# Performance work log

Hardware: AMD Instinct MI355X
Metric: run time of the kernel (lower is better)

## Reference

```python
import jax, jax.numpy as jnp
import numpy as np

LENGTH_OF_SIGNAL = 2560
OUTLIER_THRESHOLD = 3.0


def setup_inputs() -> dict:
    key = jax.random.key(0)
    inputs = jax.random.normal(key, (16384, 2560, 1), dtype=jnp.float32)
    return {"inputs": inputs}


def reference(inputs):
    # inputs: (B, S, 1). All stats reduce over the sequence axis (dim=1).
    B, S, _ = inputs.shape
    x = inputs[..., 0]  # (B, S)

    mean = jnp.mean(x, axis=1)                       # (B,)
    maximum = jnp.max(x, axis=1)
    minimum = jnp.min(x, axis=1)
    p2p = maximum - minimum
    rms = jnp.sqrt(jnp.mean(x * x, axis=1))
    var = jnp.var(x, axis=1, ddof=1)                 # torch.var is unbiased
    std = jnp.sqrt(var)                              # torch.std is unbiased

    centered = x - mean[:, None]
    skewness = jnp.mean(centered ** 3, axis=1) / (std ** 3)
    kurtosis = jnp.mean(centered ** 4, axis=1) / (std ** 4)

    abs_x = jnp.abs(x)
    abs_sum = jnp.sum(abs_x, axis=1)
    abs_max = jnp.max(abs_x, axis=1)
    shape_factor = rms * LENGTH_OF_SIGNAL / abs_sum
    impulse_factor = abs_max * LENGTH_OF_SIGNAL / abs_sum

    outliers = jnp.sum(
        (jnp.abs(centered) > OUTLIER_THRESHOLD * std[:, None]).astype(jnp.int32),
        axis=1,
    ).astype(jnp.float32)

    # zero-crossing rate on flattened (B, S) signal
    zcr = jnp.sum(
        (jnp.diff(jnp.sign(x), axis=1) != 0).astype(jnp.float32), axis=1
    ) / (2.0 * S)

    # Hjorth parameters (activity, mobility, complexity)
    d1 = jnp.diff(x, axis=1)
    d2 = jnp.diff(d1, axis=1)
    var_d1 = jnp.var(d1, axis=1, ddof=1)
    var_d2 = jnp.var(d2, axis=1, ddof=1)
    activity = var
    mobility = jnp.sqrt(var_d1 / var)
    complexity = jnp.sqrt(var_d2 / var_d1)

    stacked = jnp.stack(
        [mean, maximum, minimum, p2p, var, rms, skewness, kurtosis,
         shape_factor, impulse_factor, outliers, zcr,
         activity, mobility, complexity],
        axis=1,
    )  # (B, 15)
    return stacked
```

## Files before the change

kernel.cpp:

```cpp
#include <hip/hip_runtime.h>
#include <math.h>


typedef float f32x2 __attribute__((ext_vector_type(2)));
typedef float f32x4 __attribute__((ext_vector_type(4)));

constexpr int S_LEN = 2560;
constexpr int NROWS = 16384;

#define DPP_ADD_F32(x, ctrl) do { \
    int t_ = __builtin_amdgcn_update_dpp(0, __float_as_int(x), ctrl, 0xf, 0xf, false); \
    x += __int_as_float(t_); } while (0)
#define DPP_MAX_F32(x, ctrl) do { \
    int t_ = __builtin_amdgcn_update_dpp(__float_as_int(x), __float_as_int(x), ctrl, 0xf, 0xf, false); \
    x = fmaxf(x, __int_as_float(t_)); } while (0)
#define DPP_MIN_F32(x, ctrl) do { \
    int t_ = __builtin_amdgcn_update_dpp(__float_as_int(x), __float_as_int(x), ctrl, 0xf, 0xf, false); \
    x = fminf(x, __int_as_float(t_)); } while (0)

__device__ __forceinline__ float wave_sum_f32(float x) {
    DPP_ADD_F32(x, 0x111); DPP_ADD_F32(x, 0x112); DPP_ADD_F32(x, 0x114);
    DPP_ADD_F32(x, 0x118); DPP_ADD_F32(x, 0x142); DPP_ADD_F32(x, 0x143);
    return x;
}
__device__ __forceinline__ float wave_max_f32(float x) {
    DPP_MAX_F32(x, 0x111); DPP_MAX_F32(x, 0x112); DPP_MAX_F32(x, 0x114);
    DPP_MAX_F32(x, 0x118); DPP_MAX_F32(x, 0x142); DPP_MAX_F32(x, 0x143);
    return x;
}
__device__ __forceinline__ float wave_min_f32(float x) {
    DPP_MIN_F32(x, 0x111); DPP_MIN_F32(x, 0x112); DPP_MIN_F32(x, 0x114);
    DPP_MIN_F32(x, 0x118); DPP_MIN_F32(x, 0x142); DPP_MIN_F32(x, 0x143);
    return x;
}
__device__ __forceinline__ double wave_sum_f64(double x) {
#define DPP_ADD_F64(ctrl) do { \
    long long b_ = __double_as_longlong(x); \
    int lo_ = __builtin_amdgcn_update_dpp(0, (int)(b_ & 0xffffffffLL), ctrl, 0xf, 0xf, false); \
    int hi_ = __builtin_amdgcn_update_dpp(0, (int)(b_ >> 32), ctrl, 0xf, 0xf, false); \
    x += __longlong_as_double(((long long)hi_ << 32) | (unsigned int)lo_); } while (0)
    DPP_ADD_F64(0x111); DPP_ADD_F64(0x112); DPP_ADD_F64(0x114);
    DPP_ADD_F64(0x118); DPP_ADD_F64(0x142); DPP_ADD_F64(0x143);
#undef DPP_ADD_F64
    return x;
}
__device__ __forceinline__ double readlane_f64(double x, int l) {
    long long b = __double_as_longlong(x);
    int lo = __builtin_amdgcn_readlane((int)(b & 0xffffffffLL), l);
    int hi = __builtin_amdgcn_readlane((int)(b >> 32), l);
    return __longlong_as_double(((long long)hi << 32) | (unsigned int)lo);
}

__global__ __launch_bounds__(256, 8)
void health_pass1(const float* __restrict__ in, float* __restrict__ ws) {
    __shared__ double Lsum[4], Lsq[4];
    __shared__ float  Lnb[2][2];

    const int lane = threadIdx.x & 63;
    const int wid  = threadIdx.x >> 6;
    const int hidx = wid & 1;
    const int rsl  = wid >> 1;
    const int row  = blockIdx.x * 2 + rsl;

    const f32x4* rp = reinterpret_cast<const f32x4*>(in)
                    + (size_t)row * (S_LEN / 4) + hidx * (1280 / 4) + lane;

    f32x4 X[5];
#pragma unroll
    for (int k = 0; k < 5; ++k) X[k] = rp[k * 64];

    f32x2 sp = {0.f, 0.f}, qp = {0.f, 0.f}, sabsp = {0.f, 0.f};
    f32x2 vmaxp = {-INFINITY, -INFINITY}, vminp = {INFINITY, INFINITY};
#pragma unroll
    for (int k = 0; k < 5; ++k) {
        f32x2 lo = __builtin_shufflevector(X[k], X[k], 0, 1);
        f32x2 hi = __builtin_shufflevector(X[k], X[k], 2, 3);
        sp += lo + hi;
        qp = __builtin_elementwise_fma(lo, lo, qp);
        qp = __builtin_elementwise_fma(hi, hi, qp);
        sabsp += __builtin_elementwise_max(lo, -lo);
        sabsp += __builtin_elementwise_max(hi, -hi);
        vmaxp = __builtin_elementwise_max(vmaxp, __builtin_elementwise_max(lo, hi));
        vminp = __builtin_elementwise_min(vminp, __builtin_elementwise_min(lo, hi));
    }

    const double sum_l = (double)sp.x + (double)sp.y;
    const double sq_l  = (double)qp.x + (double)qp.y;
    const double sum_u = readlane_f64(wave_sum_f64(sum_l), 63);
    const double sq_u  = readlane_f64(wave_sum_f64(sq_l), 63);

    float sabs = wave_sum_f32(sabsp.x + sabsp.y);
    float vmax = wave_max_f32(fmaxf(vmaxp.x, vmaxp.y));
    float vmin = wave_min_f32(fminf(vminp.x, vminp.y));

    if (lane == 0) {
        Lsum[wid] = sum_u;  Lsq[wid] = sq_u;
        if (hidx == 1) { Lnb[rsl][0] = X[0][0]; Lnb[rsl][1] = X[0][1]; }
    }
    __syncthreads();
    const double tsum = Lsum[rsl * 2] + Lsum[rsl * 2 + 1];
    const double tsq  = Lsq[rsl * 2]  + Lsq[rsl * 2 + 1];

    const double mean = tsum * (1.0 / S_LEN);
    const double var  = (tsq - tsum * mean) * (1.0 / (S_LEN - 1));
    const double thr  = 3.0 * sqrt(var);
    const double bhi = mean + thr, blo = mean - thr;
    float bhi_f = (float)bhi;
    if ((double)bhi_f > bhi) bhi_f = __int_as_float(__float_as_int(bhi_f) - 1);
    float blo_f = (float)blo;
    if ((double)blo_f < blo) blo_f = __int_as_float(__float_as_int(blo_f) - 1);

    const float nbv0 = (hidx == 0) ? Lnb[rsl][0] : 0.f;
    const float nbv1 = (hidx == 0) ? Lnb[rsl][1] : 0.f;
    const float mf = (float)mean;
    const f32x2 nmf2 = {-mf, -mf};
    const unsigned long long tail_ok = (hidx == 0) ? ~0ULL : 0x7FFFFFFFFFFFFFFFULL;

    f32x2 c3p = {0.f, 0.f}, c4p = {0.f, 0.f};
    float r1 = 0.f, r2 = 0.f;
    int outc = 0, zcc = 0;
    const int nli = (lane + 1) & 63;

#pragma unroll
    for (int k = 0; k < 5; ++k) {
        const float x0 = X[k][0], x1 = X[k][1], x2v = X[k][2], x3 = X[k][3];
        const int kn = (k == 4) ? 0 : (k + 1);
        float v0 = (lane == 0) ? X[kn][0] : x0;
        float v1 = (lane == 0) ? X[kn][1] : x1;
        float n0 = __shfl(v0, nli);
        float n1 = __shfl(v1, nli);
        if (k == 4 && lane == 63) { n0 = nbv0; n1 = nbv1; }

        f32x2 lo = __builtin_shufflevector(X[k], X[k], 0, 1);
        f32x2 hi = __builtin_shufflevector(X[k], X[k], 2, 3);
        f32x2 cl = lo + nmf2, ch = hi + nmf2;
        f32x2 ql = cl * cl,  qh = ch * ch;
        c3p = __builtin_elementwise_fma(ql, cl, c3p);
        c3p = __builtin_elementwise_fma(qh, ch, c3p);
        c4p = __builtin_elementwise_fma(ql, ql, c4p);
        c4p = __builtin_elementwise_fma(qh, qh, c4p);

        outc += __popcll(__ballot(x0  > bhi_f || x0  < blo_f));
        outc += __popcll(__ballot(x1  > bhi_f || x1  < blo_f));
        outc += __popcll(__ballot(x2v > bhi_f || x2v < blo_f));
        outc += __popcll(__ballot(x3  > bhi_f || x3  < blo_f));

        const unsigned long long m0 = __ballot(x0  < 0.f);
        const unsigned long long m1 = __ballot(x1  < 0.f);
        const unsigned long long m2 = __ballot(x2v < 0.f);
        const unsigned long long m3 = __ballot(x3  < 0.f);
        const unsigned long long mn = __ballot(n0  < 0.f);
        zcc += __popcll(m0 ^ m1) + __popcll(m1 ^ m2) + __popcll(m2 ^ m3);
        zcc += __popcll((m3 ^ mn) & ((k == 4) ? tail_ok : ~0ULL));

        r1 = fmaf(x0, x1, fmaf(x1, x2v, fmaf(x2v, x3, fmaf(x3, n0, r1))));
        r2 = fmaf(x0, x2v, fmaf(x1, x3, fmaf(x2v, n0, fmaf(x3, n1, r2))));
    }

    float sabs_t = sabs;
    float c3_t   = wave_sum_f32(c3p.x + c3p.y);
    float c4_t   = wave_sum_f32(c4p.x + c4p.y);
    float r1_t   = wave_sum_f32(r1);
    float r2_t   = wave_sum_f32(r2);
    float vmax_t = vmax;
    float vmin_t = vmin;

    float ep_a, ep_b;
    if (hidx == 0) {
        ep_a = __int_as_float(__builtin_amdgcn_readlane(__float_as_int(X[0][0]), 0));
        ep_b = __int_as_float(__builtin_amdgcn_readlane(__float_as_int(X[0][1]), 0));
    } else {
        ep_a = X[4][2];  ep_b = X[4][3];
    }

    if (lane == 63) {
        double2* Wd = reinterpret_cast<double2*>(ws);
        f32x4*   Wf = reinterpret_cast<f32x4*>(ws);
        double2 dsum; dsum.x = sum_u; dsum.y = sq_u;
        Wd[(size_t)hidx * NROWS + row] = dsum;
        const size_t b = (size_t)(2 + hidx * 3) * NROWS + row;
        Wf[b]             = f32x4{sabs_t, vmax_t, vmin_t, c3_t};
        Wf[b + NROWS]     = f32x4{c4_t, r1_t, r2_t, (float)outc};
        Wf[b + 2 * NROWS] = f32x4{(float)zcc, ep_a, ep_b, 0.f};
    }
}

__global__ __launch_bounds__(256)
void health_finalize(const float* __restrict__ ws, float* __restrict__ out) {
    const int row = blockIdx.x * 256 + threadIdx.x;
    const double2* Wd = reinterpret_cast<const double2*>(ws);
    const f32x4*   Wf = reinterpret_cast<const f32x4*>(ws);

    const double2 s0 = Wd[row], s1 = Wd[NROWS + row];
    const f32x4 a0 = Wf[2 * NROWS + row], a1 = Wf[3 * NROWS + row], a2 = Wf[4 * NROWS + row];
    const f32x4 b0 = Wf[5 * NROWS + row], b1 = Wf[6 * NROWS + row], b2 = Wf[7 * NROWS + row];

    const double tsum = s0.x + s1.x;
    const double tsq  = s0.y + s1.y;
    const double mean = tsum * (1.0 / S_LEN);
    const double var  = (tsq - tsum * mean) * (1.0 / (S_LEN - 1));
    const double stdv = sqrt(var);

    const float tabs = a0[0] + b0[0];
    const float tmax = fmaxf(a0[1], b0[1]);
    const float tmin = fminf(a0[2], b0[2]);
    const float c3t  = a0[3] + b0[3];
    const float c4t  = a1[0] + b1[0];
    const double r1t = (double)a1[1] + (double)b1[1];
    const double r2t = (double)a1[2] + (double)b1[2];
    const float outt = a1[3] + b1[3];
    const float zct  = a2[0] + b2[0];
    const double e0 = (double)a2[1], e1 = (double)a2[2];
    const double e2 = (double)b2[1], e3 = (double)b2[2];

    const double rms  = sqrt(tsq * (1.0 / S_LEN));
    const double m3   = (double)c3t * (1.0 / S_LEN);
    const double m4   = (double)c4t * (1.0 / S_LEN);
    const double skew = m3 / (var * stdv);
    const double kurt = m4 / (var * var);
    const float  amax = fmaxf(fabsf(tmax), fabsf(tmin));
    const double shape   = rms * (double)S_LEN / (double)tabs;
    const double impulse = (double)amax * (double)S_LEN / (double)tabs;

    const double Q = tsq;
    const double s1q = 2.0 * Q - 2.0 * r1t - e0 * e0 - e3 * e3;
    const double s2q = 6.0 * Q - 8.0 * r1t + 2.0 * r2t
                     + 4.0 * (e0 * e1 + e2 * e3)
                     - 5.0 * e0 * e0 - e1 * e1 - e2 * e2 - 5.0 * e3 * e3;
    const double sd1 = e3 - e0;
    const double sd2 = (e3 - e2) - (e1 - e0);
    const double var1 = (s1q - sd1 * sd1 * (1.0 / (S_LEN - 1))) * (1.0 / (S_LEN - 2));
    const double var2 = (s2q - sd2 * sd2 * (1.0 / (S_LEN - 2))) * (1.0 / (S_LEN - 3));

    float* o = out + (size_t)row * 15;
    o[0]  = (float)mean;
    o[1]  = tmax;
    o[2]  = tmin;
    o[3]  = tmax - tmin;
    o[4]  = (float)var;
    o[5]  = (float)rms;
    o[6]  = (float)skew;
    o[7]  = (float)kurt;
    o[8]  = (float)shape;
    o[9]  = (float)impulse;
    o[10] = outt;
    o[11] = zct * (1.0f / (2.0f * S_LEN));
    o[12] = (float)var;
    o[13] = (float)sqrt(var1 / var);
    o[14] = (float)sqrt(var2 / var1);
}

extern "C" void kernel_launch(void* const* d_in, const int* in_sizes, int n_in,
                              void* d_out, int out_size, void* d_ws, size_t ws_size,
                              hipStream_t stream) {
    (void)in_sizes; (void)n_in; (void)ws_size; (void)out_size;
    const float* in = (const float*)d_in[0];
    float* out = (float*)d_out;
    float* ws  = (float*)d_ws;
    health_pass1<<<8192, 256, 0, stream>>>(in, ws);
    health_finalize<<<64, 256, 0, stream>>>(ws, out);
}
```

Before: 42.55 us.

## Compute raw third/fourth moments before the sync and expand central moments in finalize

Third and fourth powers are now accumulated on the raw values, and zero-crossing and lag-product accumulation moved into the first loop, before the block barrier. The finalize kernel turns the raw moments into central moments by binomial expansion in double precision. After the barrier only the outlier count, which needs the mean and std, remains. This shortens the critical path after the sync and allows more overlap with the loads. The risk is cancellation error in float raw moments, and occupancy hint drops from 8 to 6 waves.

```diff
diff --git a/kernel.cpp b/kernel.cpp
--- a/kernel.cpp
+++ b/kernel.cpp
@@ -51,7 +51,7 @@
     return __longlong_as_double(((long long)hi << 32) | (unsigned int)lo);
 }
 
-__global__ __launch_bounds__(256, 8)
+__global__ __launch_bounds__(256, 6)
 void health_pass1(const float* __restrict__ in, float* __restrict__ ws) {
     __shared__ double Lsum[4], Lsq[4];
     __shared__ float  Lnb[2][2];
@@ -70,18 +70,48 @@
     for (int k = 0; k < 5; ++k) X[k] = rp[k * 64];
 
     f32x2 sp = {0.f, 0.f}, qp = {0.f, 0.f}, sabsp = {0.f, 0.f};
+    f32x2 c3p = {0.f, 0.f}, c4p = {0.f, 0.f};
     f32x2 vmaxp = {-INFINITY, -INFINITY}, vminp = {INFINITY, INFINITY};
+    float r1 = 0.f, r2 = 0.f;
+    int zcc = 0;
+    const int nli = (lane + 1) & 63;
+
 #pragma unroll
     for (int k = 0; k < 5; ++k) {
+        const float x0 = X[k][0], x1 = X[k][1], x2v = X[k][2], x3 = X[k][3];
+        float v0, v1;
+        if (k < 4) { v0 = (lane == 0) ? X[k + 1][0] : x0;
+                     v1 = (lane == 0) ? X[k + 1][1] : x1; }
+        else       { v0 = (lane == 0) ? 0.f : x0;
+                     v1 = (lane == 0) ? 0.f : x1; }
+        const float n0 = __shfl(v0, nli);
+        const float n1 = __shfl(v1, nli);
+
         f32x2 lo = __builtin_shufflevector(X[k], X[k], 0, 1);
         f32x2 hi = __builtin_shufflevector(X[k], X[k], 2, 3);
         sp += lo + hi;
         qp = __builtin_elementwise_fma(lo, lo, qp);
         qp = __builtin_elementwise_fma(hi, hi, qp);
+        const f32x2 ql = lo * lo, qh = hi * hi;
+        c3p = __builtin_elementwise_fma(ql, lo, c3p);
+        c3p = __builtin_elementwise_fma(qh, hi, c3p);
+        c4p = __builtin_elementwise_fma(ql, ql, c4p);
+        c4p = __builtin_elementwise_fma(qh, qh, c4p);
         sabsp += __builtin_elementwise_max(lo, -lo);
         sabsp += __builtin_elementwise_max(hi, -hi);
         vmaxp = __builtin_elementwise_max(vmaxp, __builtin_elementwise_max(lo, hi));
         vminp = __builtin_elementwise_min(vminp, __builtin_elementwise_min(lo, hi));
+
+        const unsigned long long m0 = __ballot(x0  < 0.f);
+        const unsigned long long m1 = __ballot(x1  < 0.f);
+        const unsigned long long m2 = __ballot(x2v < 0.f);
+        const unsigned long long m3 = __ballot(x3  < 0.f);
+        const unsigned long long mn = __ballot(n0  < 0.f);
+        zcc += __popcll(m0 ^ m1) + __popcll(m1 ^ m2) + __popcll(m2 ^ m3);
+        zcc += __popcll((m3 ^ mn) & ((k == 4) ? 0x7FFFFFFFFFFFFFFFULL : ~0ULL));
+
+        r1 = fmaf(x0, x1, fmaf(x1, x2v, fmaf(x2v, x3, fmaf(x3, n0, r1))));
+        r2 = fmaf(x0, x2v, fmaf(x1, x3, fmaf(x2v, n0, fmaf(x3, n1, r2))));
     }
 
     const double sum_l = (double)sp.x + (double)sp.y;
@@ -89,9 +119,11 @@
     const double sum_u = readlane_f64(wave_sum_f64(sum_l), 63);
     const double sq_u  = readlane_f64(wave_sum_f64(sq_l), 63);
 
-    float sabs = wave_sum_f32(sabsp.x + sabsp.y);
-    float vmax = wave_max_f32(fmaxf(vmaxp.x, vmaxp.y));
-    float vmin = wave_min_f32(fminf(vminp.x, vminp.y));
+    const float sabs_t = wave_sum_f32(sabsp.x + sabsp.y);
+    const float c3_t   = wave_sum_f32(c3p.x + c3p.y);
+    const float c4_t   = wave_sum_f32(c4p.x + c4p.y);
+    const float vmax_t = wave_max_f32(fmaxf(vmaxp.x, vmaxp.y));
+    const float vmin_t = wave_min_f32(fminf(vminp.x, vminp.y));
 
     if (lane == 0) {
         Lsum[wid] = sum_u;  Lsq[wid] = sq_u;
@@ -110,60 +142,27 @@
     float blo_f = (float)blo;
     if ((double)blo_f < blo) blo_f = __int_as_float(__float_as_int(blo_f) - 1);
 
-    const float nbv0 = (hidx == 0) ? Lnb[rsl][0] : 0.f;
-    const float nbv1 = (hidx == 0) ? Lnb[rsl][1] : 0.f;
-    const float mf = (float)mean;
-    const f32x2 nmf2 = {-mf, -mf};
-    const unsigned long long tail_ok = (hidx == 0) ? ~0ULL : 0x7FFFFFFFFFFFFFFFULL;
-
-    f32x2 c3p = {0.f, 0.f}, c4p = {0.f, 0.f};
-    float r1 = 0.f, r2 = 0.f;
-    int outc = 0, zcc = 0;
-    const int nli = (lane + 1) & 63;
-
+    int outc = 0;
 #pragma unroll
     for (int k = 0; k < 5; ++k) {
-        const float x0 = X[k][0], x1 = X[k][1], x2v = X[k][2], x3 = X[k][3];
-        const int kn = (k == 4) ? 0 : (k + 1);
-        float v0 = (lane == 0) ? X[kn][0] : x0;
-        float v1 = (lane == 0) ? X[kn][1] : x1;
-        float n0 = __shfl(v0, nli);
-        float n1 = __shfl(v1, nli);
-        if (k == 4 && lane == 63) { n0 = nbv0; n1 = nbv1; }
-
-        f32x2 lo = __builtin_shufflevector(X[k], X[k], 0, 1);
-        f32x2 hi = __builtin_shufflevector(X[k], X[k], 2, 3);
-        f32x2 cl = lo + nmf2, ch = hi + nmf2;
-        f32x2 ql = cl * cl,  qh = ch * ch;
-        c3p = __builtin_elementwise_fma(ql, cl, c3p);
-        c3p = __builtin_elementwise_fma(qh, ch, c3p);
-        c4p = __builtin_elementwise_fma(ql, ql, c4p);
-        c4p = __builtin_elementwise_fma(qh, qh, c4p);
-
-        outc += __popcll(__ballot(x0  > bhi_f || x0  < blo_f));
-        outc += __popcll(__ballot(x1  > bhi_f || x1  < blo_f));
-        outc += __popcll(__ballot(x2v > bhi_f || x2v < blo_f));
-        outc += __popcll(__ballot(x3  > bhi_f || x3  < blo_f));
-
-        const unsigned long long m0 = __ballot(x0  < 0.f);
-        const unsigned long long m1 = __ballot(x1  < 0.f);
-        const unsigned long long m2 = __ballot(x2v < 0.f);
-        const unsigned long long m3 = __ballot(x3  < 0.f);
-        const unsigned long long mn = __ballot(n0  < 0.f);
-        zcc += __popcll(m0 ^ m1) + __popcll(m1 ^ m2) + __popcll(m2 ^ m3);
-        zcc += __popcll((m3 ^ mn) & ((k == 4) ? tail_ok : ~0ULL));
-
-        r1 = fmaf(x0, x1, fmaf(x1, x2v, fmaf(x2v, x3, fmaf(x3, n0, r1))));
-        r2 = fmaf(x0, x2v, fmaf(x1, x3, fmaf(x2v, n0, fmaf(x3, n1, r2))));
-    }
-
-    float sabs_t = sabs;
-    float c3_t   = wave_sum_f32(c3p.x + c3p.y);
-    float c4_t   = wave_sum_f32(c4p.x + c4p.y);
-    float r1_t   = wave_sum_f32(r1);
-    float r2_t   = wave_sum_f32(r2);
-    float vmax_t = vmax;
-    float vmin_t = vmin;
+        outc += __popcll(__ballot(X[k][0] > bhi_f || X[k][0] < blo_f));
+        outc += __popcll(__ballot(X[k][1] > bhi_f || X[k][1] < blo_f));
+        outc += __popcll(__ballot(X[k][2] > bhi_f || X[k][2] < blo_f));
+        outc += __popcll(__ballot(X[k][3] > bhi_f || X[k][3] < blo_f));
+    }
+
+    const float nb0 = Lnb[rsl][0], nb1 = Lnb[rsl][1];
+    int zcf = zcc;
+    if (hidx == 0) {
+        const int xe = __builtin_amdgcn_readlane(__float_as_int(X[4][3]), 63);
+        zcf += ((xe ^ __float_as_int(nb0)) < 0) ? 1 : 0;
+        if (lane == 63) {
+            r1 = fmaf(X[4][3], nb0, r1);
+            r2 = fmaf(X[4][2], nb0, fmaf(X[4][3], nb1, r2));
+        }
+    }
+    const float r1_t = wave_sum_f32(r1);
+    const float r2_t = wave_sum_f32(r2);
 
     float ep_a, ep_b;
     if (hidx == 0) {
@@ -181,7 +180,7 @@
         const size_t b = (size_t)(2 + hidx * 3) * NROWS + row;
         Wf[b]             = f32x4{sabs_t, vmax_t, vmin_t, c3_t};
         Wf[b + NROWS]     = f32x4{c4_t, r1_t, r2_t, (float)outc};
-        Wf[b + 2 * NROWS] = f32x4{(float)zcc, ep_a, ep_b, 0.f};
+        Wf[b + 2 * NROWS] = f32x4{(float)zcf, ep_a, ep_b, 0.f};
     }
 }
 
@@ -204,8 +203,8 @@
     const float tabs = a0[0] + b0[0];
     const float tmax = fmaxf(a0[1], b0[1]);
     const float tmin = fminf(a0[2], b0[2]);
-    const float c3t  = a0[3] + b0[3];
-    const float c4t  = a1[0] + b1[0];
+    const double c3raw = (double)a0[3] + (double)b0[3];
+    const double c4raw = (double)a1[0] + (double)b1[0];
     const double r1t = (double)a1[1] + (double)b1[1];
     const double r2t = (double)a1[2] + (double)b1[2];
     const float outt = a1[3] + b1[3];
@@ -213,11 +212,14 @@
     const double e0 = (double)a2[1], e1 = (double)a2[2];
     const double e2 = (double)b2[1], e3 = (double)b2[2];
 
+    const double n = (double)S_LEN;
+    const double mu2 = mean * mean;
+    const double s3 = c3raw - 3.0 * mean * tsq + 2.0 * n * mu2 * mean;
+    const double s4 = c4raw - 4.0 * mean * c3raw + 6.0 * mu2 * tsq - 3.0 * n * mu2 * mu2;
+
     const double rms  = sqrt(tsq * (1.0 / S_LEN));
-    const double m3   = (double)c3t * (1.0 / S_LEN);
-    const double m4   = (double)c4t * (1.0 / S_LEN);
-    const double skew = m3 / (var * stdv);
-    const double kurt = m4 / (var * var);
+    const double skew = (s3 * (1.0 / S_LEN)) / (var * stdv);
+    const double kurt = (s4 * (1.0 / S_LEN)) / (var * var);
     const float  amax = fmaxf(fabsf(tmax), fabsf(tmin));
     const double shape   = rms * (double)S_LEN / (double)tabs;
     const double impulse = (double)amax * (double)S_LEN / (double)tabs;
```

Result: faster. 38.92 us (-8.5%).
